# Kernel tuning notes

Hardware: AMD Instinct MI355X
Metric: run time of the kernel (lower is better)

The kernel has to match this reference:

```python
import jax, jax.numpy as jnp
import numpy as np

HID = 10
IN_DIM = 256
B, H, W = 8, 96, 96


def _conv(x, w, b=None, pad=0):
    y = jax.lax.conv_general_dilated(x, w, (1, 1), [(pad, pad), (pad, pad)],
                                     dimension_numbers=('NCHW', 'OIHW', 'NCHW'))
    return y if b is None else y + b[None, :, None, None]


def _bn(x, g, b):
    # eval-mode InPlaceABN(Sync) with identity running stats -> per-channel affine
    return x * g[None, :, None, None] + b[None, :, None, None]


def _branch(x, w1, g1, b1, w2, g2, b2):
    # Conv3x3 -> BN -> ReLU -> Conv1x1 -> BN -> ReLU  (relation / comp_u / comp_l)
    y = jax.nn.relu(_bn(_conv(x, w1, pad=1), g1, b1))
    return jax.nn.relu(_bn(_conv(y, w2), g2, b2))


def _gru(x, h, gw, gb, cw, cg, cb):
    # ConvGRU with 1x1 kernels
    gates = _conv(jnp.concatenate([x, h], axis=1), gw, gb)
    r = jax.nn.sigmoid(gates[:, 0:1])
    u = jax.nn.sigmoid(gates[:, 1:2])
    cnm = jax.nn.relu(_bn(_conv(jnp.concatenate([x, r * h], axis=1), cw), cg, cb))
    return (1.0 - u) * h + u * cnm


def setup_inputs():
    key = jax.random.key(0)
    ks = iter(jax.random.split(key, 48))

    def nrm(shape, s=0.05):
        return jax.random.normal(next(ks), shape, jnp.float32) * s

    inp = {
        'f_nodes': jax.random.normal(next(ks), (2, B, HID, H, W), jnp.float32),
        'h_nodes': jax.random.normal(next(ks), (3, B, HID, H, W), jnp.float32),
        'p_nodes': jax.random.normal(next(ks), (7, B, HID, H, W), jnp.float32),
        'xh': jax.random.normal(next(ks), (B, IN_DIM, H, W), jnp.float32),
        'f_atts': jax.random.uniform(next(ks), (2, B, 1, H, W), jnp.float32),
        'p_atts': jax.random.uniform(next(ks), (7, B, 1, H, W), jnp.float32),
        # Decomposition.decomp_att: Conv3x3(257->256)+BN+ReLU, Conv1x1(256->2)+bias
        'da_w1': nrm((IN_DIM, IN_DIM + 1, 3, 3)),
        'da_g1': jnp.ones((IN_DIM,), jnp.float32),
        'da_b1': jnp.zeros((IN_DIM,), jnp.float32),
        'da_w2': nrm((2, IN_DIM, 1, 1)),
        'da_b2': jnp.zeros((2,), jnp.float32),
    }
    # relation (shared across children), comp_u, comp_l: Conv3x3(20->10)+BN+ReLU, Conv1x1(10->10)+BN+ReLU
    for p in ('rel', 'cu', 'cl'):
        inp[p + '_w1'] = nrm((HID, 2 * HID, 3, 3))
        inp[p + '_g1'] = jnp.ones((HID,), jnp.float32)
        inp[p + '_b1'] = jnp.zeros((HID,), jnp.float32)
        inp[p + '_w2'] = nrm((HID, HID, 1, 1))
        inp[p + '_g2'] = jnp.ones((HID,), jnp.float32)
        inp[p + '_b2'] = jnp.zeros((HID,), jnp.float32)
    # 3 ConvGRUs (cls_h), 1x1 kernels, stacked on leading dim
    inp['gru_gw'] = nrm((3, 2, 2 * HID, 1, 1))
    inp['gru_gb'] = jnp.zeros((3, 2), jnp.float32)
    inp['gru_cw'] = nrm((3, HID, 2 * HID, 1, 1))
    inp['gru_cg'] = jnp.ones((3, HID), jnp.float32)
    inp['gru_cb'] = jnp.zeros((3, HID), jnp.float32)
    return inp


def reference(f_nodes, h_nodes, p_nodes, xh, f_atts, p_atts,
              da_w1, da_g1, da_b1, da_w2, da_b2,
              rel_w1, rel_g1, rel_b1, rel_w2, rel_g2, rel_b2,
              cu_w1, cu_g1, cu_b1, cu_w2, cu_g2, cu_b2,
              cl_w1, cl_g1, cl_b1, cl_w2, cl_g2, cl_b2,
              gru_gw, gru_gb, gru_cw, gru_cg, gru_cb):
    parent, parent_att = f_nodes[1], f_atts[1]
    # Decomposition of full-body node into 2 half nodes
    dm = _conv(jnp.concatenate([parent_att, xh], axis=1), da_w1, pad=1)
    dm = jax.nn.relu(_bn(dm, da_g1, da_b1))
    dm = _conv(dm, da_w2, da_b2)  # [B, 2, H, W] decomposition map
    datt = jax.nn.softmax(dm, axis=1)
    decomp = [_branch(jnp.concatenate([parent * datt[:, i:i + 1] * parent_att,
                                       h_nodes[1 + i]], axis=1),
                      rel_w1, rel_g1, rel_b1, rel_w2, rel_g2, rel_b2)
              for i in range(2)]
    # node 0: background
    n0 = _gru(f_nodes[0] + p_nodes[0], h_nodes[0],
              gru_gw[0], gru_gb[0], gru_cw[0], gru_cg[0], gru_cb[0])
    # node 1: upper half = composition(upper parts 1-4) + decomposition
    up = jnp.sum(p_nodes[1:5], axis=0) * jnp.sum(p_atts[1:5], axis=0)
    comp_u = _branch(jnp.concatenate([h_nodes[1], up], axis=1),
                     cu_w1, cu_g1, cu_b1, cu_w2, cu_g2, cu_b2)
    n1 = _gru(comp_u + decomp[0], h_nodes[1],
              gru_gw[1], gru_gb[1], gru_cw[1], gru_cg[1], gru_cb[1])
    # node 2: lower half = composition(lower parts 5-6) + decomposition
    lo = jnp.sum(p_nodes[5:7], axis=0) * jnp.sum(p_atts[5:7], axis=0)
    comp_l = _branch(jnp.concatenate([h_nodes[2], lo], axis=1),
                     cl_w1, cl_g1, cl_b1, cl_w2, cl_g2, cl_b2)
    n2 = _gru(comp_l + decomp[1], h_nodes[2],
              gru_gw[2], gru_gb[2], gru_cw[2], gru_cg[2], gru_cb[2])
    return (jnp.stack([n0, n1, n2]), dm)
```

## Files before the change

### kernel.cpp

```cpp
#include <hip/hip_runtime.h>
#include <cstddef>
#include <cstdint>

constexpr int Bn    = 8;
constexpr int Hn    = 96;
constexpr int Wn    = 96;
constexpr int HWn   = Hn * Wn;
constexpr int BHWn  = Bn * HWn;
constexpr int B10HW = Bn * 10 * HWn;

constexpr int XP_COLS        = 100;
constexpr int XP_ROWS        = 100;
constexpr int XP_PLANE       = XP_ROWS * XP_COLS;
constexpr int XP_PLANE_BYTES = XP_PLANE * 16;
constexpr int XP_OCT         = 36;

using short8  = __attribute__((ext_vector_type(8))) short;
using ushort8 = __attribute__((ext_vector_type(8))) unsigned short;
using float4v = __attribute__((ext_vector_type(4))) float;

__device__ __forceinline__ unsigned short f2bf(float f) {
    unsigned u = __builtin_bit_cast(unsigned, f);
    u += 0x7FFFu + ((u >> 16) & 1u);
    return (unsigned short)(u >> 16);
}

__device__ __forceinline__ void async16(const void* g, void* l) {
    auto gp = (__attribute__((address_space(1))) unsigned int*)(uintptr_t)g;
    auto lp = (__attribute__((address_space(3))) unsigned int*)(unsigned)(uintptr_t)l;
    __builtin_amdgcn_global_load_lds(gp, lp, 16, 0, 0);
}

struct BranchW  { const float *w1, *g1, *b1, *w2, *g2, *b2; };
struct BranchW3 { BranchW p[3]; };

constexpr int PACKW_BLOCKS = 2592;

__global__ void k_pack(const float* __restrict__ w1, short* __restrict__ wpk,
                       const float* __restrict__ xh, const float* __restrict__ patt,
                       ushort* __restrict__ xp)
{
    if (blockIdx.x < PACKW_BLOCKS) {
        const int o = blockIdx.x * 256 + threadIdx.x;
        const int j    = o & 7;
        const int lane = (o >> 3) & 63;
        const int q    = (o >> 9) & 15;
        const int t    = o >> 13;
        const int co   = q * 16 + (lane & 15);
        const int ci   = (t / 9) * 32 + ((lane >> 4) & 3) * 8 + j;
        const int tap  = t % 9;
        const float f  = (ci < 257) ? w1[((size_t)co * 257 + ci) * 9 + tap] : 0.f;
        wpk[o] = (short)f2bf(f);
    } else {
        const int g  = (blockIdx.x - PACKW_BLOCKS) * 256 + threadIdx.x;
        const int cw = g % XP_COLS;
        int t = g / XP_COLS;
        const int rh = t % XP_ROWS; t /= XP_ROWS;
        const int o  = t % XP_OCT;
        const int b  = t / XP_OCT;
        const int hh = rh - 1, ww = cw - 1;
        const bool inb = ((unsigned)hh < (unsigned)Hn) & ((unsigned)ww < (unsigned)Wn);
        const int off = hh * Wn + ww;
        ushort8 v;
        #pragma unroll
        for (int j = 0; j < 8; ++j) {
            const int ci = o * 8 + j;
            float f = 0.f;
            if (inb && ci < 257)
                f = (ci == 0) ? patt[b * HWn + off]
                              : xh[((size_t)b * 256 + (ci - 1)) * HWn + off];
            v[j] = f2bf(f);
        }
        *(ushort8*)&xp[(size_t)g * 8] = v;
    }
}

__global__ void k_packw(const float* __restrict__ w1, short* __restrict__ wpk)
{
    const int o = blockIdx.x * 256 + threadIdx.x;
    if (o >= 663552) return;
    const int j    = o & 7;
    const int lane = (o >> 3) & 63;
    const int q    = (o >> 9) & 15;
    const int t    = o >> 13;
    const int co   = q * 16 + (lane & 15);
    const int ci   = (t / 9) * 32 + ((lane >> 4) & 3) * 8 + j;
    const int tap  = t % 9;
    const float f  = (ci < 257) ? w1[((size_t)co * 257 + ci) * 9 + tap] : 0.f;
    wpk[o] = (short)f2bf(f);
}

__global__ __launch_bounds__(256, 3)
void k_bigconv3(const char* __restrict__ xp, const float* __restrict__ patt,
                const short* __restrict__ wpk, const float* __restrict__ g1,
                const float* __restrict__ b1, const float* __restrict__ w2,
                const float* __restrict__ db2,
                float* __restrict__ dm_out, float* __restrict__ s01)
{
    __shared__ __align__(16) short xs[2][4][194][8];
    __shared__ float part[4][64][2];

    const int tid  = threadIdx.x;
    const int lane = tid & 63;
    const int wid  = tid >> 6;
    const int bx   = blockIdx.x;
    const int b    = bx & 7;
    const int r2   = bx >> 3;
    const int wseg = r2 % 3;
    const int hb   = r2 / 3;
    const int h0   = hb * 2, w0 = wseg * 32;
    const int am   = lane & 15;
    const int aq   = lane >> 4;

    int poff[3];
    #pragma unroll
    for (int it = 0; it < 3; ++it) {
        const int pos = it * 64 + lane;
        const int row = pos / 34, col = pos - row * 34;
        poff[it] = ((h0 + row) * XP_COLS + (w0 + col)) * 16;
    }
    const char* xpb = xp + ((size_t)b * XP_OCT + wid) * XP_PLANE_BYTES;

    float4v acc[4][4];
    #pragma unroll
    for (int i = 0; i < 4; ++i)
        #pragma unroll
        for (int j = 0; j < 4; ++j)
            acc[i][j] = float4v{0.f, 0.f, 0.f, 0.f};

    int arow[4], acol[4];
    #pragma unroll
    for (int mt = 0; mt < 4; ++mt) {
        const int m = mt * 16 + am;
        arow[mt] = m >> 5;
        acol[mt] = m & 31;
    }

    auto stageX = [&](int cb, int buf) {
        const char* src = xpb + (size_t)cb * (4 * XP_PLANE_BYTES);
        #pragma unroll
        for (int it = 0; it < 3; ++it)
            async16(src + poff[it], &xs[buf][wid][it * 64][0]);
    };

    const short8* wp = (const short8*)wpk;
    const int qb = wid * 4;

    auto loadB = [&](int t, short8* dst) {
        #pragma unroll
        for (int nt = 0; nt < 4; ++nt)
            dst[nt] = wp[((size_t)t * 16 + qb + nt) * 64 + lane];
    };

    stageX(0, 0);
    short8 bfr[3][4];
    loadB(0, bfr[0]);
    loadB(1, bfr[1]);
    __syncthreads();

    for (int cb = 0; cb < 9; ++cb) {
        const int buf = cb & 1;
        if (cb < 8) stageX(cb + 1, buf ^ 1);
        #pragma unroll
        for (int tap = 0; tap < 9; ++tap) {
            const int t  = cb * 9 + tap;
            const int tl = (t + 2 <= 80) ? (t + 2) : 80;
            loadB(tl, bfr[(tap + 2) % 3]);
            const int kh = tap / 3, kw = tap % 3;
            short8 afr[4];
            #pragma unroll
            for (int mt = 0; mt < 4; ++mt) {
                const int pos = (arow[mt] + kh) * 34 + (acol[mt] + kw);
                afr[mt] = *(const short8*)&xs[buf][aq][pos][0];
            }
            #pragma unroll
            for (int mt = 0; mt < 4; ++mt)
                #pragma unroll
                for (int nt = 0; nt < 4; ++nt)
                    acc[mt][nt] = __builtin_amdgcn_mfma_f32_16x16x32_bf16(
                        afr[mt], bfr[tap % 3][nt], acc[mt][nt], 0, 0, 0);
        }
        __syncthreads();
    }

    float gv[4], bv[4], wa[4], wbv[4];
    #pragma unroll
    for (int nt = 0; nt < 4; ++nt) {
        const int co = wid * 64 + nt * 16 + am;
        gv[nt]  = g1[co];
        bv[nt]  = b1[co];
        wa[nt]  = w2[co];
        wbv[nt] = w2[256 + co];
    }
    #pragma unroll
    for (int mt = 0; mt < 4; ++mt) {
        #pragma unroll
        for (int reg = 0; reg < 4; ++reg) {
            float s0 = 0.f, s1 = 0.f;
            #pragma unroll
            for (int nt = 0; nt < 4; ++nt) {
                const float y = fmaxf(fmaf(acc[mt][nt][reg], gv[nt], bv[nt]), 0.f);
                s0 = fmaf(wa[nt], y, s0);
                s1 = fmaf(wbv[nt], y, s1);
            }
            #pragma unroll
            for (int off = 1; off < 16; off <<= 1) {
                s0 += __shfl_xor(s0, off, 64);
                s1 += __shfl_xor(s1, off, 64);
            }
            if (am == 0) {
                const int m = mt * 16 + aq * 4 + reg;
                part[wid][m][0] = s0;
                part[wid][m][1] = s1;
            }
        }
    }
    __syncthreads();
    if (tid < 64) {
        const int m = tid, r = m >> 5, c = m & 31;
        const int off = (h0 + r) * Wn + (w0 + c);
        float d0 = part[0][m][0] + part[1][m][0] + part[2][m][0] + part[3][m][0] + db2[0];
        float d1 = part[0][m][1] + part[1][m][1] + part[2][m][1] + part[3][m][1] + db2[1];
        dm_out[(size_t)(b * 2) * HWn + off]     = d0;
        dm_out[(size_t)(b * 2 + 1) * HWn + off] = d1;
        const float mx = fmaxf(d0, d1);
        const float e0 = expf(d0 - mx), e1 = expf(d1 - mx);
        const float pa = patt[b * HWn + off];
        const float inv = pa / (e0 + e1);
        s01[b * HWn + off]        = e0 * inv;
        s01[BHWn + b * HWn + off] = e1 * inv;
    }
}

__global__ __launch_bounds__(256, 3)
void k_bigconv3_f(const float* __restrict__ xh, const float* __restrict__ patt,
                  const short* __restrict__ wpk, const float* __restrict__ g1,
                  const float* __restrict__ b1, const float* __restrict__ w2,
                  const float* __restrict__ db2,
                  float* __restrict__ dm_out, float* __restrict__ s01)
{
    __shared__ __align__(16) short xs[2][4][137][8];
    __shared__ float part[4][64][2];

    const int tid  = threadIdx.x;
    const int lane = tid & 63;
    const int wid  = tid >> 6;
    const int bx   = blockIdx.x;
    const int b    = bx & 7;
    const int r2   = bx >> 3;
    const int wseg = r2 % 3;
    const int hb   = r2 / 3;
    const int h0   = hb * 2, w0 = wseg * 32;
    const int am   = lane & 15;
    const int aq   = lane >> 4;

    float4v acc[4][4];
    #pragma unroll
    for (int i = 0; i < 4; ++i)
        #pragma unroll
        for (int j = 0; j < 4; ++j)
            acc[i][j] = float4v{0.f, 0.f, 0.f, 0.f};

    int arow[4], acol[4];
    #pragma unroll
    for (int mt = 0; mt < 4; ++mt) {
        const int m = mt * 16 + am;
        arow[mt] = m >> 5;
        acol[mt] = m & 31;
    }

    auto stageX = [&](int cb, int buf) {
        const int cig0 = cb * 32 + wid * 8;
        for (int pos = lane; pos < 136; pos += 64) {
            const int row = pos / 34, col = pos % 34;
            const int hh = h0 - 1 + row, ww = w0 - 1 + col;
            const bool inb = ((unsigned)hh < (unsigned)Hn) & ((unsigned)ww < (unsigned)Wn);
            const int off = hh * Wn + ww;
            ushort8 v;
            #pragma unroll
            for (int j = 0; j < 8; ++j) {
                const int ci = cig0 + j;
                float f = 0.f;
                if (inb && ci < 257)
                    f = (ci == 0) ? patt[b * HWn + off]
                                  : xh[((size_t)b * 256 + (ci - 1)) * HWn + off];
                v[j] = f2bf(f);
            }
            *(ushort8*)&xs[buf][wid][pos][0] = v;
        }
    };

    const short8* wp = (const short8*)wpk;
    const int qb = wid * 4;

    stageX(0, 0);
    short8 bfr[4], bnx[4];
    #pragma unroll
    for (int nt = 0; nt < 4; ++nt)
        bfr[nt] = wp[(size_t)(qb + nt) * 64 + lane];
    __syncthreads();

    for (int cb = 0; cb < 9; ++cb) {
        const int buf = cb & 1;
        for (int tap = 0; tap < 9; ++tap) {
            const int t = cb * 9 + tap;
            if (t < 80) {
                #pragma unroll
                for (int nt = 0; nt < 4; ++nt)
                    bnx[nt] = wp[((size_t)(t + 1) * 16 + qb + nt) * 64 + lane];
            }
            const int kh = tap / 3, kw = tap % 3;
            short8 afr[4];
            #pragma unroll
            for (int mt = 0; mt < 4; ++mt) {
                const int pos = (arow[mt] + kh) * 34 + (acol[mt] + kw);
                afr[mt] = *(const short8*)&xs[buf][aq][pos][0];
            }
            #pragma unroll
            for (int mt = 0; mt < 4; ++mt)
                #pragma unroll
                for (int nt = 0; nt < 4; ++nt)
                    acc[mt][nt] = __builtin_amdgcn_mfma_f32_16x16x32_bf16(
                        afr[mt], bfr[nt], acc[mt][nt], 0, 0, 0);
            #pragma unroll
            for (int nt = 0; nt < 4; ++nt) bfr[nt] = bnx[nt];
        }
        if (cb < 8) stageX(cb + 1, buf ^ 1);
        __syncthreads();
    }

    float gv[4], bv[4], wa[4], wbv[4];
    #pragma unroll
    for (int nt = 0; nt < 4; ++nt) {
        const int co = wid * 64 + nt * 16 + am;
        gv[nt]  = g1[co];
        bv[nt]  = b1[co];
        wa[nt]  = w2[co];
        wbv[nt] = w2[256 + co];
    }
    #pragma unroll
    for (int mt = 0; mt < 4; ++mt) {
        #pragma unroll
        for (int reg = 0; reg < 4; ++reg) {
            float s0 = 0.f, s1 = 0.f;
            #pragma unroll
            for (int nt = 0; nt < 4; ++nt) {
                const float y = fmaxf(fmaf(acc[mt][nt][reg], gv[nt], bv[nt]), 0.f);
                s0 = fmaf(wa[nt], y, s0);
                s1 = fmaf(wbv[nt], y, s1);
            }
            #pragma unroll
            for (int off = 1; off < 16; off <<= 1) {
                s0 += __shfl_xor(s0, off, 64);
                s1 += __shfl_xor(s1, off, 64);
            }
            if (am == 0) {
                const int m = mt * 16 + aq * 4 + reg;
                part[wid][m][0] = s0;
                part[wid][m][1] = s1;
            }
        }
    }
    __syncthreads();
    if (tid < 64) {
        const int m = tid, r = m >> 5, c = m & 31;
        const int off = (h0 + r) * Wn + (w0 + c);
        float d0 = part[0][m][0] + part[1][m][0] + part[2][m][0] + part[3][m][0] + db2[0];
        float d1 = part[0][m][1] + part[1][m][1] + part[2][m][1] + part[3][m][1] + db2[1];
        dm_out[(size_t)(b * 2) * HWn + off]     = d0;
        dm_out[(size_t)(b * 2 + 1) * HWn + off] = d1;
        const float mx = fmaxf(d0, d1);
        const float e0 = expf(d0 - mx), e1 = expf(d1 - mx);
        const float pa = patt[b * HWn + off];
        const float inv = pa / (e0 + e1);
        s01[b * HWn + off]        = e0 * inv;
        s01[BHWn + b * HWn + off] = e1 * inv;
    }
}

__global__ __launch_bounds__(256)
void k_branch(BranchW3 P, const float* __restrict__ parent, const float* __restrict__ h_nodes,
              const float* __restrict__ s01, const float* __restrict__ pn,
              const float* __restrict__ pa, float* __restrict__ bout)
{
    const int z  = blockIdx.y;
    const int pi = (z < 2) ? 0 : (z - 1);
    __shared__ float xt[20][10][34];
    __shared__ float paSum[340];
    __shared__ __align__(16) float wlt[9 * 20 * 12];
    __shared__ float w2l[100], g1l[10], b1l[10], g2l[10], b2l[10];

    const BranchW& Pw = P.p[pi];
    const int tid = threadIdx.x;
    for (int idx = tid; idx < 2160; idx += 256) {
        const int co = idx % 12, rem = idx / 12, ci = rem % 20, tap = rem / 20;
        wlt[idx] = (co < 10) ? Pw.w1[(co * 20 + ci) * 9 + tap] : 0.f;
    }
    if (tid < 100) w2l[tid] = Pw.w2[tid];
    if (tid < 10) {
        g1l[tid] = Pw.g1[tid]; b1l[tid] = Pw.b1[tid];
        g2l[tid] = Pw.g2[tid]; b2l[tid] = Pw.b2[tid];
    }

    const int bx = blockIdx.x;
    const int tw = bx % 3, th = (bx / 3) % 12, b = bx / 36;
    const int h0 = th * 8, w0 = tw * 32;

    const float* Ab;
    const float* sc = nullptr;
    const float* Bb = nullptr;
    int k0 = 0, k1 = -1;
    if (z == 0)      { Ab = parent; sc = s01;        Bb = h_nodes + (size_t)1 * B10HW; }
    else if (z == 1) { Ab = parent; sc = s01 + BHWn; Bb = h_nodes + (size_t)2 * B10HW; }
    else if (z == 2) { Ab = h_nodes + (size_t)1 * B10HW; k0 = 1; k1 = 4; }
    else             { Ab = h_nodes + (size_t)2 * B10HW; k0 = 5; k1 = 6; }

    if (z >= 2) {
        for (int idx = tid; idx < 340; idx += 256) {
            const int col = idx % 34, row = idx / 34;
            const int hh = h0 - 1 + row, ww = w0 - 1 + col;
            float s = 0.f;
            if (((unsigned)hh < (unsigned)Hn) & ((unsigned)ww < (unsigned)Wn)) {
                const int off = hh * Wn + ww;
                for (int k = k0; k <= k1; ++k)
                    s += pa[(size_t)(k * Bn + b) * HWn + off];
            }
            paSum[idx] = s;
        }
    }
    __syncthreads();

    for (int idx = tid; idx < 6800; idx += 256) {
        const int col = idx % 34, rem = idx / 34, row = rem % 10, ch = rem / 10;
        const int hh = h0 - 1 + row, ww = w0 - 1 + col;
        float v = 0.f;
        if (((unsigned)hh < (unsigned)Hn) & ((unsigned)ww < (unsigned)Wn)) {
            const int off = hh * Wn + ww;
            if (ch < 10) {
                v = Ab[((size_t)b * 10 + ch) * HWn + off];
                if (sc) v *= sc[b * HWn + off];
            } else if (z < 2) {
                v = Bb[((size_t)b * 10 + (ch - 10)) * HWn + off];
            } else {
                float s = 0.f;
                for (int k = k0; k <= k1; ++k)
                    s += pn[((size_t)(k * Bn + b) * 10 + (ch - 10)) * HWn + off];
                v = s * paSum[row * 34 + col];
            }
        }
        ((float*)xt)[idx] = v;
    }
    __syncthreads();

    const int r = tid >> 5, c = tid & 31;
    float a0 = 0, a1 = 0, a2 = 0, a3 = 0, a4 = 0, a5 = 0, a6 = 0, a7 = 0, a8 = 0, a9 = 0;
    #pragma unroll
    for (int tap = 0; tap < 9; ++tap) {
        const int kh = tap / 3, kw = tap % 3;
        #pragma unroll
        for (int ci = 0; ci < 20; ++ci) {
            const float xv = xt[ci][r + kh][c + kw];
            const float4 wA = *(const float4*)&wlt[(tap * 20 + ci) * 12];
            const float4 wB = *(const float4*)&wlt[(tap * 20 + ci) * 12 + 4];
            const float2 wC = *(const float2*)&wlt[(tap * 20 + ci) * 12 + 8];
            a0 = fmaf(wA.x, xv, a0); a1 = fmaf(wA.y, xv, a1);
            a2 = fmaf(wA.z, xv, a2); a3 = fmaf(wA.w, xv, a3);
            a4 = fmaf(wB.x, xv, a4); a5 = fmaf(wB.y, xv, a5);
            a6 = fmaf(wB.z, xv, a6); a7 = fmaf(wB.w, xv, a7);
            a8 = fmaf(wC.x, xv, a8); a9 = fmaf(wC.y, xv, a9);
        }
    }
    float acc[10] = {a0, a1, a2, a3, a4, a5, a6, a7, a8, a9};
    float y[10];
    #pragma unroll
    for (int co = 0; co < 10; ++co)
        y[co] = fmaxf(fmaf(acc[co], g1l[co], b1l[co]), 0.f);
    const int hw = (h0 + r) * Wn + (w0 + c);
    #pragma unroll
    for (int co = 0; co < 10; ++co) {
        float s = 0.f;
        #pragma unroll
        for (int i = 0; i < 10; ++i) s = fmaf(w2l[co * 10 + i], y[i], s);
        s = fmaxf(fmaf(s, g2l[co], b2l[co]), 0.f);
        bout[(size_t)z * B10HW + ((size_t)b * 10 + co) * HWn + hw] = s;
    }
}

__global__ void k_gru(const float* __restrict__ f_nodes, const float* __restrict__ h_nodes,
                      const float* __restrict__ p_nodes, const float* __restrict__ bout,
                      const float* __restrict__ gw, const float* __restrict__ gb,
                      const float* __restrict__ cw, const float* __restrict__ cg,
                      const float* __restrict__ cb, float* __restrict__ out)
{
    const int z = blockIdx.y;
    __shared__ float gwl[40], cwl[200], gbl[2], cgl[10], cbl[10];
    if (threadIdx.x < 40)  gwl[threadIdx.x] = gw[z * 40 + threadIdx.x];
    if (threadIdx.x < 200) cwl[threadIdx.x] = cw[z * 200 + threadIdx.x];
    if (threadIdx.x < 2)   gbl[threadIdx.x] = gb[z * 2 + threadIdx.x];
    if (threadIdx.x < 10) {
        cgl[threadIdx.x] = cg[z * 10 + threadIdx.x];
        cbl[threadIdx.x] = cb[z * 10 + threadIdx.x];
    }
    __syncthreads();

    const int p = blockIdx.x * 256 + threadIdx.x;
    const int b = p / HWn, hw = p % HWn;
    float x[10], h[10];
    #pragma unroll
    for (int c = 0; c < 10; ++c) {
        const size_t idx = ((size_t)b * 10 + c) * HWn + hw;
        if (z == 0)      x[c] = f_nodes[idx] + p_nodes[idx];
        else if (z == 1) x[c] = bout[(size_t)2 * B10HW + idx] + bout[idx];
        else             x[c] = bout[(size_t)3 * B10HW + idx] + bout[(size_t)1 * B10HW + idx];
        h[c] = h_nodes[(size_t)z * B10HW + idx];
    }
    float g0 = gbl[0], g1 = gbl[1];
    #pragma unroll
    for (int c = 0; c < 10; ++c) {
        g0 = fmaf(gwl[c],      x[c], g0);
        g0 = fmaf(gwl[10 + c], h[c], g0);
        g1 = fmaf(gwl[20 + c], x[c], g1);
        g1 = fmaf(gwl[30 + c], h[c], g1);
    }
    const float r = 1.f / (1.f + expf(-g0));
    const float u = 1.f / (1.f + expf(-g1));
    #pragma unroll
    for (int o = 0; o < 10; ++o) {
        float s = 0.f;
        #pragma unroll
        for (int c = 0; c < 10; ++c) {
            s = fmaf(cwl[o * 20 + c],      x[c],     s);
            s = fmaf(cwl[o * 20 + 10 + c], r * h[c], s);
        }
        s = fmaxf(fmaf(s, cgl[o], cbl[o]), 0.f);
        out[(size_t)z * B10HW + ((size_t)b * 10 + o) * HWn + hw] =
            (1.f - u) * h[o] + u * s;
    }
}

extern "C" void kernel_launch(void* const* d_in, const int* in_sizes, int n_in,
                              void* d_out, int out_size, void* d_ws, size_t ws_size,
                              hipStream_t stream)
{
    (void)in_sizes; (void)n_in; (void)out_size;

    const float* f_nodes = (const float*)d_in[0];
    const float* h_nodes = (const float*)d_in[1];
    const float* p_nodes = (const float*)d_in[2];
    const float* xh      = (const float*)d_in[3];
    const float* f_atts  = (const float*)d_in[4];
    const float* p_atts  = (const float*)d_in[5];
    const float* da_w1   = (const float*)d_in[6];
    const float* da_g1   = (const float*)d_in[7];
    const float* da_b1   = (const float*)d_in[8];
    const float* da_w2   = (const float*)d_in[9];
    const float* da_b2   = (const float*)d_in[10];

    BranchW3 P;
    for (int i = 0; i < 3; ++i) {
        P.p[i].w1 = (const float*)d_in[11 + 6 * i + 0];
        P.p[i].g1 = (const float*)d_in[11 + 6 * i + 1];
        P.p[i].b1 = (const float*)d_in[11 + 6 * i + 2];
        P.p[i].w2 = (const float*)d_in[11 + 6 * i + 3];
        P.p[i].g2 = (const float*)d_in[11 + 6 * i + 4];
        P.p[i].b2 = (const float*)d_in[11 + 6 * i + 5];
    }
    const float* gru_gw = (const float*)d_in[29];
    const float* gru_gb = (const float*)d_in[30];
    const float* gru_cw = (const float*)d_in[31];
    const float* gru_cg = (const float*)d_in[32];
    const float* gru_cb = (const float*)d_in[33];

    float* out    = (float*)d_out;
    float* dm_out = out + (size_t)3 * B10HW;

    float* ws   = (float*)d_ws;
    float* s01  = ws;
    float* bout = s01 + 2 * BHWn;
    short* wpk  = (short*)bout;
    const size_t XP_OFF_B = ((size_t)(2 * BHWn) + 4 * (size_t)B10HW) * 4;
    char*  xp   = (char*)d_ws + XP_OFF_B;
    const size_t WS_NEED = XP_OFF_B + (size_t)Bn * XP_OCT * XP_PLANE_BYTES;
    const bool use_packed = ws_size >= WS_NEED;

    const float* patt   = f_atts + BHWn;
    const float* parent = f_nodes + B10HW;

    if (use_packed) {
        k_pack<<<dim3(PACKW_BLOCKS + 11250), 256, 0, stream>>>(da_w1, wpk, xh, patt,
                                                               (ushort*)xp);
        k_bigconv3<<<dim3(1152), 256, 0, stream>>>(xp, patt, wpk, da_g1, da_b1,
                                                   da_w2, da_b2, dm_out, s01);
    } else {
        k_packw<<<dim3(2592), 256, 0, stream>>>(da_w1, wpk);
        k_bigconv3_f<<<dim3(1152), 256, 0, stream>>>(xh, patt, wpk, da_g1, da_b1,
                                                     da_w2, da_b2, dm_out, s01);
    }
    k_branch<<<dim3(288, 4), 256, 0, stream>>>(P, parent, h_nodes, s01,
                                               p_nodes, p_atts, bout);
    k_gru<<<dim3(288, 3), 256, 0, stream>>>(f_nodes, h_nodes, p_nodes, bout,
                                            gru_gw, gru_gb, gru_cw, gru_cg, gru_cb, out);
}
```

Baseline: 374.4 us.

## Double-buffer A/B fragments in big conv; two output rows per thread in branch

The big MFMA conv loop now ping-pongs both A fragments (from LDS) and B fragments (weights) one tap ahead instead of keeping a three-deep B ring and loading A just before use. The intent is to hide LDS read latency behind the MFMA block. Separately, the branch conv tile grows from 8 to 16 rows, so each thread computes two output rows and reuses each loaded weight for both. That halves the grid and the relative halo overhead, but raises register and LDS use and leaves fewer blocks.

```diff
diff --git a/kernel.cpp b/kernel.cpp
--- a/kernel.cpp
+++ b/kernel.cpp
@@ -146,39 +146,56 @@
     const short8* wp = (const short8*)wpk;
     const int qb = wid * 4;
 
-    auto loadB = [&](int t, short8* dst) {
+    auto loadB = [&](int t, short8 (&dst)[4]) {
         #pragma unroll
         for (int nt = 0; nt < 4; ++nt)
             dst[nt] = wp[((size_t)t * 16 + qb + nt) * 64 + lane];
     };
+    auto loadA = [&](int buf, int tap, short8 (&dst)[4]) {
+        const int kh = tap / 3, kw = tap % 3;
+        #pragma unroll
+        for (int mt = 0; mt < 4; ++mt) {
+            const int pos = (arow[mt] + kh) * 34 + (acol[mt] + kw);
+            dst[mt] = *(const short8*)&xs[buf][aq][pos][0];
+        }
+    };
+    auto mfmaBlk = [&](short8 (&afr)[4], short8 (&bfr)[4]) {
+        #pragma unroll
+        for (int mt = 0; mt < 4; ++mt)
+            #pragma unroll
+            for (int nt = 0; nt < 4; ++nt)
+                acc[mt][nt] = __builtin_amdgcn_mfma_f32_16x16x32_bf16(
+                    afr[mt], bfr[nt], acc[mt][nt], 0, 0, 0);
+    };
+
+    short8 bfrA[4], bfrB[4], afrA[4], afrB[4];
 
     stageX(0, 0);
-    short8 bfr[3][4];
-    loadB(0, bfr[0]);
-    loadB(1, bfr[1]);
+    loadB(0, bfrA);
     __syncthreads();
 
     for (int cb = 0; cb < 9; ++cb) {
         const int buf = cb & 1;
         if (cb < 8) stageX(cb + 1, buf ^ 1);
+        loadA(buf, 0, afrA);
         #pragma unroll
         for (int tap = 0; tap < 9; ++tap) {
-            const int t  = cb * 9 + tap;
-            const int tl = (t + 2 <= 80) ? (t + 2) : 80;
-            loadB(tl, bfr[(tap + 2) % 3]);
-            const int kh = tap / 3, kw = tap % 3;
-            short8 afr[4];
-            #pragma unroll
-            for (int mt = 0; mt < 4; ++mt) {
-                const int pos = (arow[mt] + kh) * 34 + (acol[mt] + kw);
-                afr[mt] = *(const short8*)&xs[buf][aq][pos][0];
-            }
-            #pragma unroll
-            for (int mt = 0; mt < 4; ++mt)
-                #pragma unroll
-                for (int nt = 0; nt < 4; ++nt)
-                    acc[mt][nt] = __builtin_amdgcn_mfma_f32_16x16x32_bf16(
-                        afr[mt], bfr[tap % 3][nt], acc[mt][nt], 0, 0, 0);
+            const int t = cb * 9 + tap;
+            if ((tap & 1) == 0) {
+                if (tap < 8) {
+                    loadB(t + 1, bfrB);
+                    loadA(buf, tap + 1, afrB);
+                }
+                mfmaBlk(afrA, bfrA);
+                if (tap == 8) {
+                    const int tn = (t + 1 <= 80) ? (t + 1) : 80;
+                    loadB(tn, bfrA);
+                }
+            } else {
+                loadB(t + 1, bfrA);
+                loadA(buf, tap + 1, afrA);
+                mfmaBlk(afrB, bfrB);
+            }
         }
         __syncthreads();
     }
@@ -385,8 +402,8 @@
 {
     const int z  = blockIdx.y;
     const int pi = (z < 2) ? 0 : (z - 1);
-    __shared__ float xt[20][10][34];
-    __shared__ float paSum[340];
+    __shared__ float xt[20][18][34];
+    __shared__ float paSum[612];
     __shared__ __align__(16) float wlt[9 * 20 * 12];
     __shared__ float w2l[100], g1l[10], b1l[10], g2l[10], b2l[10];
 
@@ -403,8 +420,8 @@
     }
 
     const int bx = blockIdx.x;
-    const int tw = bx % 3, th = (bx / 3) % 12, b = bx / 36;
-    const int h0 = th * 8, w0 = tw * 32;
+    const int tw = bx % 3, th = (bx / 3) % 6, b = bx / 18;
+    const int h0 = th * 16, w0 = tw * 32;
 
     const float* Ab;
     const float* sc = nullptr;
@@ -416,7 +433,7 @@
     else             { Ab = h_nodes + (size_t)2 * B10HW; k0 = 5; k1 = 6; }
 
     if (z >= 2) {
-        for (int idx = tid; idx < 340; idx += 256) {
+        for (int idx = tid; idx < 612; idx += 256) {
             const int col = idx % 34, row = idx / 34;
             const int hh = h0 - 1 + row, ww = w0 - 1 + col;
             float s = 0.f;
@@ -430,8 +447,8 @@
     }
     __syncthreads();
 
-    for (int idx = tid; idx < 6800; idx += 256) {
-        const int col = idx % 34, rem = idx / 34, row = rem % 10, ch = rem / 10;
+    for (int idx = tid; idx < 12240; idx += 256) {
+        const int col = idx % 34, rem = idx / 34, row = rem % 18, ch = rem / 18;
         const int hh = h0 - 1 + row, ww = w0 - 1 + col;
         float v = 0.f;
         if (((unsigned)hh < (unsigned)Hn) & ((unsigned)ww < (unsigned)Wn)) {
@@ -453,36 +470,46 @@
     __syncthreads();
 
     const int r = tid >> 5, c = tid & 31;
-    float a0 = 0, a1 = 0, a2 = 0, a3 = 0, a4 = 0, a5 = 0, a6 = 0, a7 = 0, a8 = 0, a9 = 0;
+    float acc0[10] = {0,0,0,0,0,0,0,0,0,0};
+    float acc1[10] = {0,0,0,0,0,0,0,0,0,0};
     #pragma unroll
     for (int tap = 0; tap < 9; ++tap) {
         const int kh = tap / 3, kw = tap % 3;
         #pragma unroll
         for (int ci = 0; ci < 20; ++ci) {
-            const float xv = xt[ci][r + kh][c + kw];
+            const float xv0 = xt[ci][r + kh][c + kw];
+            const float xv1 = xt[ci][r + 8 + kh][c + kw];
             const float4 wA = *(const float4*)&wlt[(tap * 20 + ci) * 12];
             const float4 wB = *(const float4*)&wlt[(tap * 20 + ci) * 12 + 4];
             const float2 wC = *(const float2*)&wlt[(tap * 20 + ci) * 12 + 8];
-            a0 = fmaf(wA.x, xv, a0); a1 = fmaf(wA.y, xv, a1);
-            a2 = fmaf(wA.z, xv, a2); a3 = fmaf(wA.w, xv, a3);
-            a4 = fmaf(wB.x, xv, a4); a5 = fmaf(wB.y, xv, a5);
-            a6 = fmaf(wB.z, xv, a6); a7 = fmaf(wB.w, xv, a7);
-            a8 = fmaf(wC.x, xv, a8); a9 = fmaf(wC.y, xv, a9);
-        }
-    }
-    float acc[10] = {a0, a1, a2, a3, a4, a5, a6, a7, a8, a9};
-    float y[10];
-    #pragma unroll
-    for (int co = 0; co < 10; ++co)
-        y[co] = fmaxf(fmaf(acc[co], g1l[co], b1l[co]), 0.f);
-    const int hw = (h0 + r) * Wn + (w0 + c);
-    #pragma unroll
-    for (int co = 0; co < 10; ++co) {
-        float s = 0.f;
-        #pragma unroll
-        for (int i = 0; i < 10; ++i) s = fmaf(w2l[co * 10 + i], y[i], s);
-        s = fmaxf(fmaf(s, g2l[co], b2l[co]), 0.f);
-        bout[(size_t)z * B10HW + ((size_t)b * 10 + co) * HWn + hw] = s;
+            acc0[0] = fmaf(wA.x, xv0, acc0[0]); acc1[0] = fmaf(wA.x, xv1, acc1[0]);
+            acc0[1] = fmaf(wA.y, xv0, acc0[1]); acc1[1] = fmaf(wA.y, xv1, acc1[1]);
+            acc0[2] = fmaf(wA.z, xv0, acc0[2]); acc1[2] = fmaf(wA.z, xv1, acc1[2]);
+            acc0[3] = fmaf(wA.w, xv0, acc0[3]); acc1[3] = fmaf(wA.w, xv1, acc1[3]);
+            acc0[4] = fmaf(wB.x, xv0, acc0[4]); acc1[4] = fmaf(wB.x, xv1, acc1[4]);
+            acc0[5] = fmaf(wB.y, xv0, acc0[5]); acc1[5] = fmaf(wB.y, xv1, acc1[5]);
+            acc0[6] = fmaf(wB.z, xv0, acc0[6]); acc1[6] = fmaf(wB.z, xv1, acc1[6]);
+            acc0[7] = fmaf(wB.w, xv0, acc0[7]); acc1[7] = fmaf(wB.w, xv1, acc1[7]);
+            acc0[8] = fmaf(wC.x, xv0, acc0[8]); acc1[8] = fmaf(wC.x, xv1, acc1[8]);
+            acc0[9] = fmaf(wC.y, xv0, acc0[9]); acc1[9] = fmaf(wC.y, xv1, acc1[9]);
+        }
+    }
+    #pragma unroll
+    for (int px = 0; px < 2; ++px) {
+        float* ac = px ? acc1 : acc0;
+        float y[10];
+        #pragma unroll
+        for (int co = 0; co < 10; ++co)
+            y[co] = fmaxf(fmaf(ac[co], g1l[co], b1l[co]), 0.f);
+        const int hw = (h0 + r + px * 8) * Wn + (w0 + c);
+        #pragma unroll
+        for (int co = 0; co < 10; ++co) {
+            float s = 0.f;
+            #pragma unroll
+            for (int i = 0; i < 10; ++i) s = fmaf(w2l[co * 10 + i], y[i], s);
+            s = fmaxf(fmaf(s, g2l[co], b2l[co]), 0.f);
+            bout[(size_t)z * B10HW + ((size_t)b * 10 + co) * HWn + hw] = s;
+        }
     }
 }
 
@@ -596,7 +623,7 @@
         k_bigconv3_f<<<dim3(1152), 256, 0, stream>>>(xh, patt, wpk, da_g1, da_b1,
                                                      da_w2, da_b2, dm_out, s01);
     }
-    k_branch<<<dim3(288, 4), 256, 0, stream>>>(P, parent, h_nodes, s01,
+    k_branch<<<dim3(144, 4), 256, 0, stream>>>(P, parent, h_nodes, s01,
                                                p_nodes, p_atts, bout);
     k_gru<<<dim3(288, 3), 256, 0, stream>>>(f_nodes, h_nodes, p_nodes, bout,
                                             gru_gw, gru_gb, gru_cw, gru_cg, gru_cb, out);
```

Result: slower. 449.4 us (+20.0%).

## Double output tile rows per block in packed 3x3 conv to reuse weights

Applied to the files above, without the earlier changes.

The packed big-conv kernel now computes 4 output rows by 32 columns per block instead of 2, doubling the M tiles per wave (8 accumulator sets) and halving the grid to 576 blocks. Each loaded weight fragment now feeds twice as many MFMAs, which reduces global weight traffic per output. The weight prefetch drops from a 3-deep ring to a single-step double buffer, and the tap loop is no longer unrolled. In exchange, register pressure rises (launch bounds drop from 3 to 2 waves per SIMD), LDS use grows, and fewer blocks are available to fill the GPU.

```diff
diff --git a/kernel.cpp b/kernel.cpp
--- a/kernel.cpp
+++ b/kernel.cpp
@@ -90,15 +90,17 @@
     wpk[o] = (short)f2bf(f);
 }
 
-__global__ __launch_bounds__(256, 3)
+constexpr int XS_STRIDE = 258;
+
+__global__ __launch_bounds__(256, 2)
 void k_bigconv3(const char* __restrict__ xp, const float* __restrict__ patt,
                 const short* __restrict__ wpk, const float* __restrict__ g1,
                 const float* __restrict__ b1, const float* __restrict__ w2,
                 const float* __restrict__ db2,
                 float* __restrict__ dm_out, float* __restrict__ s01)
 {
-    __shared__ __align__(16) short xs[2][4][194][8];
-    __shared__ float part[4][64][2];
+    __shared__ __align__(16) short xs[2][4][XS_STRIDE][8];
+    __shared__ float part[4][128][2];
 
     const int tid  = threadIdx.x;
     const int lane = tid & 63;
@@ -108,29 +110,29 @@
     const int r2   = bx >> 3;
     const int wseg = r2 % 3;
     const int hb   = r2 / 3;
-    const int h0   = hb * 2, w0 = wseg * 32;
+    const int h0   = hb * 4, w0 = wseg * 32;
     const int am   = lane & 15;
     const int aq   = lane >> 4;
 
-    int poff[3];
-    #pragma unroll
-    for (int it = 0; it < 3; ++it) {
+    int poff[4];
+    #pragma unroll
+    for (int it = 0; it < 4; ++it) {
         const int pos = it * 64 + lane;
         const int row = pos / 34, col = pos - row * 34;
         poff[it] = ((h0 + row) * XP_COLS + (w0 + col)) * 16;
     }
     const char* xpb = xp + ((size_t)b * XP_OCT + wid) * XP_PLANE_BYTES;
 
-    float4v acc[4][4];
-    #pragma unroll
-    for (int i = 0; i < 4; ++i)
+    float4v acc[8][4];
+    #pragma unroll
+    for (int i = 0; i < 8; ++i)
         #pragma unroll
         for (int j = 0; j < 4; ++j)
             acc[i][j] = float4v{0.f, 0.f, 0.f, 0.f};
 
-    int arow[4], acol[4];
-    #pragma unroll
-    for (int mt = 0; mt < 4; ++mt) {
+    int arow[8], acol[8];
+    #pragma unroll
+    for (int mt = 0; mt < 8; ++mt) {
         const int m = mt * 16 + am;
         arow[mt] = m >> 5;
         acol[mt] = m & 31;
@@ -139,46 +141,49 @@
     auto stageX = [&](int cb, int buf) {
         const char* src = xpb + (size_t)cb * (4 * XP_PLANE_BYTES);
         #pragma unroll
-        for (int it = 0; it < 3; ++it)
+        for (int it = 0; it < 4; ++it)
             async16(src + poff[it], &xs[buf][wid][it * 64][0]);
     };
 
     const short8* wp = (const short8*)wpk;
     const int qb = wid * 4;
 
-    auto loadB = [&](int t, short8* dst) {
-        #pragma unroll
-        for (int nt = 0; nt < 4; ++nt)
-            dst[nt] = wp[((size_t)t * 16 + qb + nt) * 64 + lane];
-    };
-
     stageX(0, 0);
-    short8 bfr[3][4];
-    loadB(0, bfr[0]);
-    loadB(1, bfr[1]);
+    short8 bfr[4], bnx[4];
+    #pragma unroll
+    for (int nt = 0; nt < 4; ++nt)
+        bfr[nt] = wp[(size_t)(qb + nt) * 64 + lane];
     __syncthreads();
 
     for (int cb = 0; cb < 9; ++cb) {
         const int buf = cb & 1;
         if (cb < 8) stageX(cb + 1, buf ^ 1);
-        #pragma unroll
         for (int tap = 0; tap < 9; ++tap) {
-            const int t  = cb * 9 + tap;
-            const int tl = (t + 2 <= 80) ? (t + 2) : 80;
-            loadB(tl, bfr[(tap + 2) % 3]);
-            const int kh = tap / 3, kw = tap % 3;
-            short8 afr[4];
-            #pragma unroll
-            for (int mt = 0; mt < 4; ++mt) {
-                const int pos = (arow[mt] + kh) * 34 + (acol[mt] + kw);
-                afr[mt] = *(const short8*)&xs[buf][aq][pos][0];
-            }
-            #pragma unroll
-            for (int mt = 0; mt < 4; ++mt)
+            const int t = cb * 9 + tap;
+            if (t < 80) {
                 #pragma unroll
                 for (int nt = 0; nt < 4; ++nt)
-                    acc[mt][nt] = __builtin_amdgcn_mfma_f32_16x16x32_bf16(
-                        afr[mt], bfr[tap % 3][nt], acc[mt][nt], 0, 0, 0);
+                    bnx[nt] = wp[((size_t)(t + 1) * 16 + qb + nt) * 64 + lane];
+            }
+            const int kh = tap / 3, kw = tap % 3;
+            #pragma unroll
+            for (int mh = 0; mh < 2; ++mh) {
+                short8 afr[4];
+                #pragma unroll
+                for (int mi = 0; mi < 4; ++mi) {
+                    const int mt = mh * 4 + mi;
+                    const int pos = (arow[mt] + kh) * 34 + (acol[mt] + kw);
+                    afr[mi] = *(const short8*)&xs[buf][aq][pos][0];
+                }
+                #pragma unroll
+                for (int mi = 0; mi < 4; ++mi)
+                    #pragma unroll
+                    for (int nt = 0; nt < 4; ++nt)
+                        acc[mh * 4 + mi][nt] = __builtin_amdgcn_mfma_f32_16x16x32_bf16(
+                            afr[mi], bfr[nt], acc[mh * 4 + mi][nt], 0, 0, 0);
+            }
+            #pragma unroll
+            for (int nt = 0; nt < 4; ++nt) bfr[nt] = bnx[nt];
         }
         __syncthreads();
     }
@@ -193,7 +198,7 @@
         wbv[nt] = w2[256 + co];
     }
     #pragma unroll
-    for (int mt = 0; mt < 4; ++mt) {
+    for (int mt = 0; mt < 8; ++mt) {
         #pragma unroll
         for (int reg = 0; reg < 4; ++reg) {
             float s0 = 0.f, s1 = 0.f;
@@ -216,7 +221,7 @@
         }
     }
     __syncthreads();
-    if (tid < 64) {
+    if (tid < 128) {
         const int m = tid, r = m >> 5, c = m & 31;
         const int off = (h0 + r) * Wn + (w0 + c);
         float d0 = part[0][m][0] + part[1][m][0] + part[2][m][0] + part[3][m][0] + db2[0];
@@ -589,8 +594,8 @@
     if (use_packed) {
         k_pack<<<dim3(PACKW_BLOCKS + 11250), 256, 0, stream>>>(da_w1, wpk, xh, patt,
                                                                (ushort*)xp);
-        k_bigconv3<<<dim3(1152), 256, 0, stream>>>(xp, patt, wpk, da_g1, da_b1,
-                                                   da_w2, da_b2, dm_out, s01);
+        k_bigconv3<<<dim3(576), 256, 0, stream>>>(xp, patt, wpk, da_g1, da_b1,
+                                                  da_w2, da_b2, dm_out, s01);
     } else {
         k_packw<<<dim3(2592), 256, 0, stream>>>(da_w1, wpk);
         k_bigconv3_f<<<dim3(1152), 256, 0, stream>>>(xh, patt, wpk, da_g1, da_b1,
```

Result: slower. 385.8 us (+3.0%).
